# Optimization experiments

Hardware: AMD Instinct MI355X
Metric: run time of the kernel (lower is better)

The kernel has to match this reference:

```python
import jax, jax.numpy as jnp
import numpy as np
import math

B, C_IN, H, W = 8, 256, 32, 32
KDIM, OUT_CH, NUM_HEADS = 512, 512, 8


def setup_inputs() -> dict:
    key = jax.random.key(0)
    ks = jax.random.split(key, 7)
    s = 1.0 / math.sqrt(C_IN)
    inp = {
        "input": jax.random.normal(ks[0], (B, C_IN, H, W), dtype=jnp.float32),
        "q_w": jax.random.uniform(ks[1], (KDIM, C_IN), jnp.float32, -s, s),
        "q_b": jax.random.uniform(ks[2], (KDIM,), jnp.float32, -s, s),
        "k_w": jax.random.uniform(ks[3], (KDIM, C_IN), jnp.float32, -s, s),
        "k_b": jax.random.uniform(ks[4], (KDIM,), jnp.float32, -s, s),
        "v_w": jax.random.uniform(ks[5], (OUT_CH, C_IN), jnp.float32, -s, s),
        "v_b": jax.random.uniform(ks[6], (OUT_CH,), jnp.float32, -s, s),
    }
    return inp


def reference(input, q_w, q_b, k_w, k_b, v_w, v_b):
    b, c, h, w = input.shape
    s = h * w
    hd_k = KDIM // NUM_HEADS
    hd_v = OUT_CH // NUM_HEADS
    # (b, c, h, w) -> (b, s, c)
    x = jnp.transpose(input, (0, 2, 3, 1)).reshape(b, s, c)
    q = x @ q_w.T + q_b  # (b, s, kdim)
    k = x @ k_w.T + k_b  # (b, s, kdim)
    v = x @ v_w.T + v_b  # (b, s, out_ch)
    q = q.reshape(b, s, NUM_HEADS, hd_k).transpose(0, 2, 1, 3)  # (b, nh, s, hd)
    k = k.reshape(b, s, NUM_HEADS, hd_k).transpose(0, 2, 1, 3)
    v = v.reshape(b, s, NUM_HEADS, hd_v).transpose(0, 2, 1, 3)
    scores = jnp.einsum("bhqd,bhkd->bhqk", q, k) / math.sqrt(hd_k)
    causal = jnp.triu(jnp.full((s, s), -jnp.inf, dtype=scores.dtype), k=1)
    scores = scores + causal
    attn = jax.nn.softmax(scores, axis=-1)  # dropout p=0.0 -> identity
    out = jnp.einsum("bhqk,bhkd->bhqd", attn, v)  # (b, nh, s, hd_v)
    # permute(0,1,3,2) then view(b, out_ch, h, w) as in torch code
    out = out.transpose(0, 1, 3, 2).reshape(b, OUT_CH, h, w)
    return out
```

## Files before the change

### kernel.cpp

```cpp
#include <hip/hip_runtime.h>
#include <math.h>

#define BATCH 8
#define CIN 256
#define S 1024
#define KDIM 512
#define NH 8
#define HD 64

typedef float  f32x4  __attribute__((ext_vector_type(4)));
typedef short  bf16x8 __attribute__((ext_vector_type(8)));
typedef unsigned short u16x8 __attribute__((ext_vector_type(8)));

static __device__ __forceinline__ unsigned short f2bf(float x) {
    unsigned u = __builtin_bit_cast(unsigned, x);
    u += 0x7FFFu + ((u >> 16) & 1u);
    return (unsigned short)(u >> 16);
}
static __device__ __forceinline__ float bf2f(unsigned short v) {
    unsigned u = ((unsigned)v) << 16;
    return __builtin_bit_cast(float, u);
}
static __device__ __forceinline__ f32x4 mfma16(bf16x8 a, bf16x8 b, f32x4 c) {
    return __builtin_amdgcn_mfma_f32_16x16x32_bf16(a, b, c, 0, 0, 0);
}

#define PA_HI 0
#define PA_LO 8192
#define PB_HI 16384
#define PB_LO 24576

__global__ __launch_bounds__(256)
void proj_mfma_kernel(const float* __restrict__ in,
                      const float* __restrict__ q_w, const float* __restrict__ q_b,
                      const float* __restrict__ k_w, const float* __restrict__ k_b,
                      const float* __restrict__ v_w, const float* __restrict__ v_b,
                      unsigned short* __restrict__ qhi, unsigned short* __restrict__ qlo,
                      unsigned short* __restrict__ khi, unsigned short* __restrict__ klo,
                      unsigned short* __restrict__ vhi, unsigned short* __restrict__ vlo)
{
    __shared__ __attribute__((aligned(16))) char smem[32768];

    const int s0  = blockIdx.x * 128;
    const int nt  = blockIdx.y;
    const int b   = blockIdx.z;
    const int p   = nt >> 2;
    const int nb0 = (nt & 3) * 128;

    const float* w  = (p == 0) ? q_w : (p == 1) ? k_w : v_w;
    const float* bs = (p == 0) ? q_b : (p == 1) ? k_b : v_b;
    unsigned short* ph_g = (p == 0) ? qhi : (p == 1) ? khi : vhi;
    unsigned short* pl_g = (p == 0) ? qlo : (p == 1) ? klo : vlo;

    const int tid = threadIdx.x;
    const int wv  = tid >> 6;
    const int wm  = wv >> 1, wn = wv & 1;
    const int l   = tid & 63;
    const int lg  = l >> 4;
    const int lm  = l & 15;

    const float* inb = in + (size_t)b * CIN * S;

    f32x4 acc[4][4];
    #pragma unroll
    for (int mf = 0; mf < 4; ++mf)
        #pragma unroll
        for (int nf = 0; nf < 4; ++nf) acc[mf][nf] = (f32x4){0.f, 0.f, 0.f, 0.f};

    for (int c0 = 0; c0 < CIN; c0 += 32) {
        __syncthreads();
        #pragma unroll
        for (int j = 0; j < 2; ++j) {
            const int cell = tid + j * 256;
            const int m  = cell & 127;
            const int kg = cell >> 7;
            const float* src = inb + (size_t)(c0 + kg * 8) * S + s0 + m;
            u16x8 hv, lv;
            #pragma unroll
            for (int e = 0; e < 8; ++e) {
                const float v = src[(size_t)e * S];
                const unsigned short h = f2bf(v);
                hv[e] = h;
                lv[e] = f2bf(v - bf2f(h));
            }
            const int idx = (kg * 1024 + m * 8) * 2;
            *(u16x8*)(smem + PA_HI + idx) = hv;
            *(u16x8*)(smem + PA_LO + idx) = lv;
        }
        #pragma unroll
        for (int j = 0; j < 2; ++j) {
            const int cell = tid + j * 256;
            const int n  = cell & 127;
            const int kg = cell >> 7;
            const float* src = w + (size_t)(nb0 + n) * CIN + c0 + kg * 8;
            const float4 w0 = *(const float4*)src;
            const float4 w1 = *(const float4*)(src + 4);
            const float vv[8] = {w0.x, w0.y, w0.z, w0.w, w1.x, w1.y, w1.z, w1.w};
            u16x8 hv, lv;
            #pragma unroll
            for (int e = 0; e < 8; ++e) {
                const unsigned short h = f2bf(vv[e]);
                hv[e] = h;
                lv[e] = f2bf(vv[e] - bf2f(h));
            }
            const int idx = (kg * 1024 + n * 8) * 2;
            *(u16x8*)(smem + PB_HI + idx) = hv;
            *(u16x8*)(smem + PB_LO + idx) = lv;
        }
        __syncthreads();

        bf16x8 ah[4], al[4];
        #pragma unroll
        for (int mf = 0; mf < 4; ++mf) {
            const int idx = (lg * 1024 + (wm * 64 + mf * 16 + lm) * 8) * 2;
            ah[mf] = *(const bf16x8*)(smem + PA_HI + idx);
            al[mf] = *(const bf16x8*)(smem + PA_LO + idx);
        }
        __builtin_amdgcn_s_setprio(1);
        #pragma unroll
        for (int nf = 0; nf < 4; ++nf) {
            const int idx = (lg * 1024 + (wn * 64 + nf * 16 + lm) * 8) * 2;
            const bf16x8 bh = *(const bf16x8*)(smem + PB_HI + idx);
            const bf16x8 bl = *(const bf16x8*)(smem + PB_LO + idx);
            #pragma unroll
            for (int mf = 0; mf < 4; ++mf) {
                acc[mf][nf] = mfma16(ah[mf], bh, acc[mf][nf]);
                acc[mf][nf] = mfma16(al[mf], bh, acc[mf][nf]);
                acc[mf][nf] = mfma16(ah[mf], bl, acc[mf][nf]);
            }
        }
        __builtin_amdgcn_s_setprio(0);
    }

    #pragma unroll
    for (int nf = 0; nf < 4; ++nf) {
        const int ncol = nb0 + wn * 64 + nf * 16 + lm;
        const int h = ncol >> 6, d = ncol & 63;
        const float bias = bs[ncol];
        const size_t hb = ((size_t)b * NH + h) * S * HD + d;
        #pragma unroll
        for (int mf = 0; mf < 4; ++mf) {
            #pragma unroll
            for (int r = 0; r < 4; ++r) {
                const int srow = s0 + wm * 64 + mf * 16 + lg * 4 + r;
                const float x = acc[mf][nf][r] + bias;
                const unsigned short hq = f2bf(x);
                const unsigned short lq = f2bf(x - bf2f(hq));
                ph_g[hb + (size_t)srow * HD] = hq;
                pl_g[hb + (size_t)srow * HD] = lq;
            }
        }
    }
}

#define KHI_OFF  0
#define KLO_OFF  8192
#define VTHI_OFF 16384
#define VTLO_OFF 24576
#define PSHI_OFF 32768
#define PSLO_OFF 40960

__global__ __launch_bounds__(256)
void attn_mfma_kernel(const unsigned short* __restrict__ qhi_g,
                      const unsigned short* __restrict__ qlo_g,
                      const unsigned short* __restrict__ khi_g,
                      const unsigned short* __restrict__ klo_g,
                      const unsigned short* __restrict__ vhi_g,
                      const unsigned short* __restrict__ vlo_g,
                      float* __restrict__ out)
{
    __shared__ __attribute__((aligned(16))) char smem[49152];

    const int qt = 15 - (int)blockIdx.x;
    const int h  = blockIdx.y;
    const int b  = blockIdx.z;
    const int tid = threadIdx.x;
    const int w  = tid >> 6;
    const int l  = tid & 63;
    const int lg = l >> 4;
    const int lm = l & 15;
    const int s0 = qt * 64;

    const size_t base = ((size_t)b * NH + h) * S * HD;

    bf16x8 qh[2], ql[2];
    {
        const size_t qoff = base + (size_t)(s0 + w * 16 + lm) * HD + lg * 8;
        qh[0] = *(const bf16x8*)(qhi_g + qoff);
        qh[1] = *(const bf16x8*)(qhi_g + qoff + 32);
        ql[0] = *(const bf16x8*)(qlo_g + qoff);
        ql[1] = *(const bf16x8*)(qlo_g + qoff + 32);
    }

    float m[4] = {-1e30f, -1e30f, -1e30f, -1e30f};
    float lsum[4] = {0.f, 0.f, 0.f, 0.f};
    f32x4 accO[4];
    #pragma unroll
    for (int dt = 0; dt < 4; ++dt) accO[dt] = (f32x4){0.f, 0.f, 0.f, 0.f};

    for (int kt = 0; kt <= qt; ++kt) {
        __syncthreads();
        {
            const size_t kbase = base + (size_t)(kt * 64) * HD;
            #pragma unroll
            for (int i = 0; i < 2; ++i) {
                const int c = tid + i * 256;
                const int krow = c >> 3;
                const int d0 = (c & 7) * 8;
                const int swzk = (krow & 7) << 4;
                const size_t goff = kbase + (size_t)krow * HD + d0;
                const uint4 hk = *(const uint4*)(khi_g + goff);
                const uint4 lk = *(const uint4*)(klo_g + goff);
                *(uint4*)(smem + KHI_OFF + krow * 128 + ((d0 * 2) ^ swzk)) = hk;
                *(uint4*)(smem + KLO_OFF + krow * 128 + ((d0 * 2) ^ swzk)) = lk;
                const uint4 hv = *(const uint4*)(vhi_g + goff);
                const uint4 lv = *(const uint4*)(vlo_g + goff);
                const unsigned short* he = (const unsigned short*)&hv;
                const unsigned short* le = (const unsigned short*)&lv;
                #pragma unroll
                for (int j = 0; j < 8; ++j) {
                    const int d = d0 + j;
                    const int swzv = (((d >> 3) ^ d) & 7) << 4;
                    const int boff = d * 128 + ((2 * krow) ^ swzv);
                    *(unsigned short*)(smem + VTHI_OFF + boff) = he[j];
                    *(unsigned short*)(smem + VTLO_OFF + boff) = le[j];
                }
            }
        }
        __syncthreads();

        f32x4 sc[4];
        __builtin_amdgcn_s_setprio(1);
        #pragma unroll
        for (int kb = 0; kb < 4; ++kb) {
            f32x4 a = (f32x4){0.f, 0.f, 0.f, 0.f};
            #pragma unroll
            for (int ks = 0; ks < 2; ++ks) {
                const int row = kb * 16 + lm;
                const int cb = 64 * ks + 16 * lg;
                const int swz = (row & 7) << 4;
                const bf16x8 bh_ = *(const bf16x8*)(smem + KHI_OFF + row * 128 + (cb ^ swz));
                const bf16x8 bl_ = *(const bf16x8*)(smem + KLO_OFF + row * 128 + (cb ^ swz));
                a = mfma16(qh[ks], bh_, a);
                a = mfma16(ql[ks], bh_, a);
                a = mfma16(qh[ks], bl_, a);
            }
            sc[kb] = a;
        }
        __builtin_amdgcn_s_setprio(0);

        const bool diag = (kt == qt);
        float tmax[4] = {-1e30f, -1e30f, -1e30f, -1e30f};
        #pragma unroll
        for (int kb = 0; kb < 4; ++kb) {
            const int key = kt * 64 + kb * 16 + lm;
            #pragma unroll
            for (int r = 0; r < 4; ++r) {
                float v = sc[kb][r] * 0.125f;
                const int row = s0 + w * 16 + lg * 4 + r;
                if (diag && key > row) v = -1e30f;
                sc[kb][r] = v;
                tmax[r] = fmaxf(tmax[r], v);
            }
        }
        #pragma unroll
        for (int mk = 1; mk < 16; mk <<= 1)
            #pragma unroll
            for (int r = 0; r < 4; ++r)
                tmax[r] = fmaxf(tmax[r], __shfl_xor(tmax[r], mk));

        float tsum[4], sscale[4];
        #pragma unroll
        for (int r = 0; r < 4; ++r) {
            const float mn = fmaxf(m[r], tmax[r]);
            sscale[r] = __expf(m[r] - mn);
            m[r] = mn;
            float ssum = 0.f;
            #pragma unroll
            for (int kb = 0; kb < 4; ++kb) {
                const float p = __expf(sc[kb][r] - mn);
                sc[kb][r] = p;
                ssum += p;
            }
            tsum[r] = ssum;
        }
        #pragma unroll
        for (int mk = 1; mk < 16; mk <<= 1)
            #pragma unroll
            for (int r = 0; r < 4; ++r)
                tsum[r] += __shfl_xor(tsum[r], mk);

        #pragma unroll
        for (int r = 0; r < 4; ++r) {
            lsum[r] = lsum[r] * sscale[r] + tsum[r];
            #pragma unroll
            for (int dt = 0; dt < 4; ++dt) accO[dt][r] *= sscale[r];
            const int r_loc = lg * 4 + r;
            const int swz = (r_loc & 7) << 4;
            #pragma unroll
            for (int kb = 0; kb < 4; ++kb) {
                const float p = sc[kb][r];
                const unsigned short phq = f2bf(p);
                const unsigned short plq = f2bf(p - bf2f(phq));
                const int boff = (w << 11) + r_loc * 128 + ((2 * (kb * 16 + lm)) ^ swz);
                *(unsigned short*)(smem + PSHI_OFF + boff) = phq;
                *(unsigned short*)(smem + PSLO_OFF + boff) = plq;
            }
        }

        __builtin_amdgcn_s_setprio(1);
        #pragma unroll
        for (int ks = 0; ks < 2; ++ks) {
            const int cb = 64 * ks + 16 * lg;
            const int swzp = (lm & 7) << 4;
            const bf16x8 phi = *(const bf16x8*)(smem + PSHI_OFF + (w << 11) + lm * 128 + (cb ^ swzp));
            const bf16x8 plo = *(const bf16x8*)(smem + PSLO_OFF + (w << 11) + lm * 128 + (cb ^ swzp));
            #pragma unroll
            for (int dt = 0; dt < 4; ++dt) {
                const int d = dt * 16 + lm;
                const int swzv = (((d >> 3) ^ d) & 7) << 4;
                const bf16x8 vh_ = *(const bf16x8*)(smem + VTHI_OFF + d * 128 + (cb ^ swzv));
                const bf16x8 vl_ = *(const bf16x8*)(smem + VTLO_OFF + d * 128 + (cb ^ swzv));
                accO[dt] = mfma16(phi, vh_, accO[dt]);
                accO[dt] = mfma16(plo, vh_, accO[dt]);
                accO[dt] = mfma16(phi, vl_, accO[dt]);
            }
        }
        __builtin_amdgcn_s_setprio(0);
    }

    __syncthreads();
    float* Ot = (float*)smem;
    float invl[4];
    #pragma unroll
    for (int r = 0; r < 4; ++r) invl[r] = 1.0f / lsum[r];
    #pragma unroll
    for (int dt = 0; dt < 4; ++dt)
        #pragma unroll
        for (int r = 0; r < 4; ++r)
            Ot[(w * 16 + lg * 4 + r) * 66 + dt * 16 + lm] = accO[dt][r] * invl[r];
    __syncthreads();
    float* op = out + ((size_t)b * KDIM + (size_t)h * HD) * S + s0;
    #pragma unroll
    for (int i = 0; i < 16; ++i) {
        const int lin = tid + i * 256;
        const int d = lin >> 6, s = lin & 63;
        op[(size_t)d * S + s] = Ot[s * 66 + d];
    }
}

extern "C" void kernel_launch(void* const* d_in, const int* in_sizes, int n_in,
                              void* d_out, int out_size, void* d_ws, size_t ws_size,
                              hipStream_t stream)
{
    const float* input = (const float*)d_in[0];
    const float* q_w   = (const float*)d_in[1];
    const float* q_b   = (const float*)d_in[2];
    const float* k_w   = (const float*)d_in[3];
    const float* k_b   = (const float*)d_in[4];
    const float* v_w   = (const float*)d_in[5];
    const float* v_b   = (const float*)d_in[6];
    float* out = (float*)d_out;

    const size_t per = (size_t)BATCH * NH * S * HD;
    unsigned short* qhi = (unsigned short*)d_ws;
    unsigned short* qlo = qhi + per;
    unsigned short* khi = qlo + per;
    unsigned short* klo = khi + per;
    unsigned short* vhi = klo + per;
    unsigned short* vlo = vhi + per;

    proj_mfma_kernel<<<dim3(8, 12, BATCH), 256, 0, stream>>>(
        input, q_w, q_b, k_w, k_b, v_w, v_b, qhi, qlo, khi, klo, vhi, vlo);

    attn_mfma_kernel<<<dim3(S / 64, NH, BATCH), 256, 0, stream>>>(
        qhi, qlo, khi, klo, vhi, vlo, out);
}
```

Baseline: 205.6 us.

## Pre-split inputs to bf16, pair causal tiles per block, prefetch K/V

New kernels split x and the weights into bf16 hi/lo once, in a tile-friendly layout, using the output buffer as scratch. The projection then reads MFMA operands straight from global memory and no longer converts through LDS every k-step. The attention kernel gives each block two query tiles (bx and 15-bx) to balance causal work. It also register-prefetches the next K/V tile while the current one is computed. The trade-offs are extra launches, global-load latency in the projection, and reliance on the output buffer being large enough for the scratch data.

```diff
diff --git a/kernel.cpp b/kernel.cpp
--- a/kernel.cpp
+++ b/kernel.cpp
@@ -25,29 +25,94 @@
     return __builtin_amdgcn_mfma_f32_16x16x32_bf16(a, b, c, 0, 0, 0);
 }
 
-#define PA_HI 0
-#define PA_LO 8192
-#define PB_HI 16384
-#define PB_LO 24576
-
 __global__ __launch_bounds__(256)
-void proj_mfma_kernel(const float* __restrict__ in,
-                      const float* __restrict__ q_w, const float* __restrict__ q_b,
-                      const float* __restrict__ k_w, const float* __restrict__ k_b,
-                      const float* __restrict__ v_w, const float* __restrict__ v_b,
+void convert_x_kernel(const float* __restrict__ in,
+                      unsigned short* __restrict__ xt_hi,
+                      unsigned short* __restrict__ xt_lo)
+{
+    __shared__ unsigned short Hs[32][132];
+    __shared__ unsigned short Ls[32][132];
+    const int s0 = blockIdx.x * 128;
+    const int kb = blockIdx.y;
+    const int b  = blockIdx.z;
+    const int tid = threadIdx.x;
+    const float* src = in + ((size_t)b * CIN + kb * 32) * S;
+    #pragma unroll
+    for (int it = 0; it < 16; ++it) {
+        const int lin = it * 256 + tid;
+        const int c = lin >> 7;
+        const int s = lin & 127;
+        const float v = src[(size_t)c * S + s0 + s];
+        const unsigned short h = f2bf(v);
+        Hs[c][s] = h;
+        Ls[c][s] = f2bf(v - bf2f(h));
+    }
+    __syncthreads();
+    const size_t obase = ((size_t)b * 8 + kb) * (size_t)S * 32;
+    #pragma unroll
+    for (int it = 0; it < 2; ++it) {
+        const int lin = it * 256 + tid;
+        const int j = lin >> 2;
+        const int q = lin & 3;
+        u16x8 hv, lv;
+        #pragma unroll
+        for (int e = 0; e < 8; ++e) {
+            hv[e] = Hs[q * 8 + e][j];
+            lv[e] = Ls[q * 8 + e][j];
+        }
+        const size_t o = obase + (size_t)(s0 + j) * 32 + q * 8;
+        *(u16x8*)(xt_hi + o) = hv;
+        *(u16x8*)(xt_lo + o) = lv;
+    }
+}
+
+__global__ __launch_bounds__(256)
+void convert_w_kernel(const float* __restrict__ q_w, const float* __restrict__ k_w,
+                      const float* __restrict__ v_w,
+                      unsigned short* __restrict__ wt_hi,
+                      unsigned short* __restrict__ wt_lo)
+{
+    const int t = blockIdx.x * 256 + threadIdx.x;
+    const int n1536 = t >> 5;
+    const int c0 = (t & 31) * 8;
+    const int p = n1536 >> 9;
+    const int n = n1536 & 511;
+    const int kb = c0 >> 5;
+    const int cc = c0 & 31;
+    const float* w = (p == 0) ? q_w : (p == 1) ? k_w : v_w;
+    const float* src = w + (size_t)n * CIN + c0;
+    const float4 a = *(const float4*)src;
+    const float4 bq = *(const float4*)(src + 4);
+    const float vv[8] = {a.x, a.y, a.z, a.w, bq.x, bq.y, bq.z, bq.w};
+    u16x8 hv, lv;
+    #pragma unroll
+    for (int e = 0; e < 8; ++e) {
+        const unsigned short h = f2bf(vv[e]);
+        hv[e] = h;
+        lv[e] = f2bf(vv[e] - bf2f(h));
+    }
+    const size_t o = ((size_t)((p * 8 + kb) * 512 + n)) * 32 + cc;
+    *(u16x8*)(wt_hi + o) = hv;
+    *(u16x8*)(wt_lo + o) = lv;
+}
+
+__global__ __launch_bounds__(256)
+void proj_mfma_kernel(const unsigned short* __restrict__ xt_hi,
+                      const unsigned short* __restrict__ xt_lo,
+                      const unsigned short* __restrict__ wt_hi,
+                      const unsigned short* __restrict__ wt_lo,
+                      const float* __restrict__ q_b, const float* __restrict__ k_b,
+                      const float* __restrict__ v_b,
                       unsigned short* __restrict__ qhi, unsigned short* __restrict__ qlo,
                       unsigned short* __restrict__ khi, unsigned short* __restrict__ klo,
                       unsigned short* __restrict__ vhi, unsigned short* __restrict__ vlo)
 {
-    __shared__ __attribute__((aligned(16))) char smem[32768];
-
     const int s0  = blockIdx.x * 128;
     const int nt  = blockIdx.y;
     const int b   = blockIdx.z;
     const int p   = nt >> 2;
     const int nb0 = (nt & 3) * 128;
 
-    const float* w  = (p == 0) ? q_w : (p == 1) ? k_w : v_w;
     const float* bs = (p == 0) ? q_b : (p == 1) ? k_b : v_b;
     unsigned short* ph_g = (p == 0) ? qhi : (p == 1) ? khi : vhi;
     unsigned short* pl_g = (p == 0) ? qlo : (p == 1) ? klo : vlo;
@@ -59,69 +124,26 @@
     const int lg  = l >> 4;
     const int lm  = l & 15;
 
-    const float* inb = in + (size_t)b * CIN * S;
-
     f32x4 acc[4][4];
     #pragma unroll
     for (int mf = 0; mf < 4; ++mf)
         #pragma unroll
         for (int nf = 0; nf < 4; ++nf) acc[mf][nf] = (f32x4){0.f, 0.f, 0.f, 0.f};
 
-    for (int c0 = 0; c0 < CIN; c0 += 32) {
-        __syncthreads();
-        #pragma unroll
-        for (int j = 0; j < 2; ++j) {
-            const int cell = tid + j * 256;
-            const int m  = cell & 127;
-            const int kg = cell >> 7;
-            const float* src = inb + (size_t)(c0 + kg * 8) * S + s0 + m;
-            u16x8 hv, lv;
-            #pragma unroll
-            for (int e = 0; e < 8; ++e) {
-                const float v = src[(size_t)e * S];
-                const unsigned short h = f2bf(v);
-                hv[e] = h;
-                lv[e] = f2bf(v - bf2f(h));
-            }
-            const int idx = (kg * 1024 + m * 8) * 2;
-            *(u16x8*)(smem + PA_HI + idx) = hv;
-            *(u16x8*)(smem + PA_LO + idx) = lv;
-        }
-        #pragma unroll
-        for (int j = 0; j < 2; ++j) {
-            const int cell = tid + j * 256;
-            const int n  = cell & 127;
-            const int kg = cell >> 7;
-            const float* src = w + (size_t)(nb0 + n) * CIN + c0 + kg * 8;
-            const float4 w0 = *(const float4*)src;
-            const float4 w1 = *(const float4*)(src + 4);
-            const float vv[8] = {w0.x, w0.y, w0.z, w0.w, w1.x, w1.y, w1.z, w1.w};
-            u16x8 hv, lv;
-            #pragma unroll
-            for (int e = 0; e < 8; ++e) {
-                const unsigned short h = f2bf(vv[e]);
-                hv[e] = h;
-                lv[e] = f2bf(vv[e] - bf2f(h));
-            }
-            const int idx = (kg * 1024 + n * 8) * 2;
-            *(u16x8*)(smem + PB_HI + idx) = hv;
-            *(u16x8*)(smem + PB_LO + idx) = lv;
-        }
-        __syncthreads();
-
+    for (int kb = 0; kb < 8; ++kb) {
+        const size_t aoff = ((size_t)(b * 8 + kb) * S + (s0 + wm * 64 + lm)) * 32 + lg * 8;
         bf16x8 ah[4], al[4];
         #pragma unroll
         for (int mf = 0; mf < 4; ++mf) {
-            const int idx = (lg * 1024 + (wm * 64 + mf * 16 + lm) * 8) * 2;
-            ah[mf] = *(const bf16x8*)(smem + PA_HI + idx);
-            al[mf] = *(const bf16x8*)(smem + PA_LO + idx);
-        }
+            ah[mf] = *(const bf16x8*)(xt_hi + aoff + (size_t)mf * 512);
+            al[mf] = *(const bf16x8*)(xt_lo + aoff + (size_t)mf * 512);
+        }
+        const size_t boff = ((size_t)((p * 8 + kb) * 512) + (nb0 + wn * 64 + lm)) * 32 + lg * 8;
         __builtin_amdgcn_s_setprio(1);
         #pragma unroll
         for (int nf = 0; nf < 4; ++nf) {
-            const int idx = (lg * 1024 + (wn * 64 + nf * 16 + lm) * 8) * 2;
-            const bf16x8 bh = *(const bf16x8*)(smem + PB_HI + idx);
-            const bf16x8 bl = *(const bf16x8*)(smem + PB_LO + idx);
+            const bf16x8 bh = *(const bf16x8*)(wt_hi + boff + (size_t)nf * 512);
+            const bf16x8 bl = *(const bf16x8*)(wt_lo + boff + (size_t)nf * 512);
             #pragma unroll
             for (int mf = 0; mf < 4; ++mf) {
                 acc[mf][nf] = mfma16(ah[mf], bh, acc[mf][nf]);
@@ -171,7 +193,7 @@
 {
     __shared__ __attribute__((aligned(16))) char smem[49152];
 
-    const int qt = 15 - (int)blockIdx.x;
+    const int bx = blockIdx.x;
     const int h  = blockIdx.y;
     const int b  = blockIdx.z;
     const int tid = threadIdx.x;
@@ -179,44 +201,53 @@
     const int l  = tid & 63;
     const int lg = l >> 4;
     const int lm = l & 15;
-    const int s0 = qt * 64;
 
     const size_t base = ((size_t)b * NH + h) * S * HD;
 
-    bf16x8 qh[2], ql[2];
-    {
-        const size_t qoff = base + (size_t)(s0 + w * 16 + lm) * HD + lg * 8;
-        qh[0] = *(const bf16x8*)(qhi_g + qoff);
-        qh[1] = *(const bf16x8*)(qhi_g + qoff + 32);
-        ql[0] = *(const bf16x8*)(qlo_g + qoff);
-        ql[1] = *(const bf16x8*)(qlo_g + qoff + 32);
-    }
-
-    float m[4] = {-1e30f, -1e30f, -1e30f, -1e30f};
-    float lsum[4] = {0.f, 0.f, 0.f, 0.f};
-    f32x4 accO[4];
-    #pragma unroll
-    for (int dt = 0; dt < 4; ++dt) accO[dt] = (f32x4){0.f, 0.f, 0.f, 0.f};
-
-    for (int kt = 0; kt <= qt; ++kt) {
-        __syncthreads();
+    for (int pi = 0; pi < 2; ++pi) {
+        const int qt = pi ? 15 - bx : bx;
+        const int s0 = qt * 64;
+
+        bf16x8 qh[2], ql[2];
         {
-            const size_t kbase = base + (size_t)(kt * 64) * HD;
+            const size_t qoff = base + (size_t)(s0 + w * 16 + lm) * HD + lg * 8;
+            qh[0] = *(const bf16x8*)(qhi_g + qoff);
+            qh[1] = *(const bf16x8*)(qhi_g + qoff + 32);
+            ql[0] = *(const bf16x8*)(qlo_g + qoff);
+            ql[1] = *(const bf16x8*)(qlo_g + qoff + 32);
+        }
+
+        float m[4] = {-1e30f, -1e30f, -1e30f, -1e30f};
+        float lsum[4] = {0.f, 0.f, 0.f, 0.f};
+        f32x4 accO[4];
+        #pragma unroll
+        for (int dt = 0; dt < 4; ++dt) accO[dt] = (f32x4){0.f, 0.f, 0.f, 0.f};
+
+        uint4 hk[2], lk[2], hv[2], lv[2];
+        #pragma unroll
+        for (int i = 0; i < 2; ++i) {
+            const int c = tid + i * 256;
+            const int krow = c >> 3;
+            const int d0 = (c & 7) * 8;
+            const size_t goff = base + (size_t)krow * HD + d0;
+            hk[i] = *(const uint4*)(khi_g + goff);
+            lk[i] = *(const uint4*)(klo_g + goff);
+            hv[i] = *(const uint4*)(vhi_g + goff);
+            lv[i] = *(const uint4*)(vlo_g + goff);
+        }
+
+        for (int kt = 0; kt <= qt; ++kt) {
+            __syncthreads();
             #pragma unroll
             for (int i = 0; i < 2; ++i) {
                 const int c = tid + i * 256;
                 const int krow = c >> 3;
                 const int d0 = (c & 7) * 8;
                 const int swzk = (krow & 7) << 4;
-                const size_t goff = kbase + (size_t)krow * HD + d0;
-                const uint4 hk = *(const uint4*)(khi_g + goff);
-                const uint4 lk = *(const uint4*)(klo_g + goff);
-                *(uint4*)(smem + KHI_OFF + krow * 128 + ((d0 * 2) ^ swzk)) = hk;
-                *(uint4*)(smem + KLO_OFF + krow * 128 + ((d0 * 2) ^ swzk)) = lk;
-                const uint4 hv = *(const uint4*)(vhi_g + goff);
-                const uint4 lv = *(const uint4*)(vlo_g + goff);
-                const unsigned short* he = (const unsigned short*)&hv;
-                const unsigned short* le = (const unsigned short*)&lv;
+                *(uint4*)(smem + KHI_OFF + krow * 128 + ((d0 * 2) ^ swzk)) = hk[i];
+                *(uint4*)(smem + KLO_OFF + krow * 128 + ((d0 * 2) ^ swzk)) = lk[i];
+                const unsigned short* he = (const unsigned short*)&hv[i];
+                const unsigned short* le = (const unsigned short*)&lv[i];
                 #pragma unroll
                 for (int j = 0; j < 8; ++j) {
                     const int d = d0 + j;
@@ -226,126 +257,141 @@
                     *(unsigned short*)(smem + VTLO_OFF + boff) = le[j];
                 }
             }
-        }
+            if (kt < qt) {
+                const size_t kbase = base + (size_t)((kt + 1) * 64) * HD;
+                #pragma unroll
+                for (int i = 0; i < 2; ++i) {
+                    const int c = tid + i * 256;
+                    const int krow = c >> 3;
+                    const int d0 = (c & 7) * 8;
+                    const size_t goff = kbase + (size_t)krow * HD + d0;
+                    hk[i] = *(const uint4*)(khi_g + goff);
+                    lk[i] = *(const uint4*)(klo_g + goff);
+                    hv[i] = *(const uint4*)(vhi_g + goff);
+                    lv[i] = *(const uint4*)(vlo_g + goff);
+                }
+            }
+            __syncthreads();
+
+            f32x4 sc[4];
+            __builtin_amdgcn_s_setprio(1);
+            #pragma unroll
+            for (int kb = 0; kb < 4; ++kb) {
+                f32x4 a = (f32x4){0.f, 0.f, 0.f, 0.f};
+                #pragma unroll
+                for (int ks = 0; ks < 2; ++ks) {
+                    const int row = kb * 16 + lm;
+                    const int cb = 64 * ks + 16 * lg;
+                    const int swz = (row & 7) << 4;
+                    const bf16x8 bh_ = *(const bf16x8*)(smem + KHI_OFF + row * 128 + (cb ^ swz));
+                    const bf16x8 bl_ = *(const bf16x8*)(smem + KLO_OFF + row * 128 + (cb ^ swz));
+                    a = mfma16(qh[ks], bh_, a);
+                    a = mfma16(ql[ks], bh_, a);
+                    a = mfma16(qh[ks], bl_, a);
+                }
+                sc[kb] = a;
+            }
+            __builtin_amdgcn_s_setprio(0);
+
+            const bool diag = (kt == qt);
+            float tmax[4] = {-1e30f, -1e30f, -1e30f, -1e30f};
+            #pragma unroll
+            for (int kb = 0; kb < 4; ++kb) {
+                const int key = kt * 64 + kb * 16 + lm;
+                #pragma unroll
+                for (int r = 0; r < 4; ++r) {
+                    float v = sc[kb][r] * 0.125f;
+                    const int row = s0 + w * 16 + lg * 4 + r;
+                    if (diag && key > row) v = -1e30f;
+                    sc[kb][r] = v;
+                    tmax[r] = fmaxf(tmax[r], v);
+                }
+            }
+            #pragma unroll
+            for (int mk = 1; mk < 16; mk <<= 1)
+                #pragma unroll
+                for (int r = 0; r < 4; ++r)
+                    tmax[r] = fmaxf(tmax[r], __shfl_xor(tmax[r], mk));
+
+            float tsum[4], sscale[4];
+            #pragma unroll
+            for (int r = 0; r < 4; ++r) {
+                const float mn = fmaxf(m[r], tmax[r]);
+                sscale[r] = __expf(m[r] - mn);
+                m[r] = mn;
+                float ssum = 0.f;
+                #pragma unroll
+                for (int kb = 0; kb < 4; ++kb) {
+                    const float p = __expf(sc[kb][r] - mn);
+                    sc[kb][r] = p;
+                    ssum += p;
+                }
+                tsum[r] = ssum;
+            }
+            #pragma unroll
+            for (int mk = 1; mk < 16; mk <<= 1)
+                #pragma unroll
+                for (int r = 0; r < 4; ++r)
+                    tsum[r] += __shfl_xor(tsum[r], mk);
+
+            #pragma unroll
+            for (int r = 0; r < 4; ++r) {
+                lsum[r] = lsum[r] * sscale[r] + tsum[r];
+                #pragma unroll
+                for (int dt = 0; dt < 4; ++dt) accO[dt][r] *= sscale[r];
+                const int r_loc = lg * 4 + r;
+                const int swz = (r_loc & 7) << 4;
+                #pragma unroll
+                for (int kb = 0; kb < 4; ++kb) {
+                    const float p = sc[kb][r];
+                    const unsigned short phq = f2bf(p);
+                    const unsigned short plq = f2bf(p - bf2f(phq));
+                    const int boff = (w << 11) + r_loc * 128 + ((2 * (kb * 16 + lm)) ^ swz);
+                    *(unsigned short*)(smem + PSHI_OFF + boff) = phq;
+                    *(unsigned short*)(smem + PSLO_OFF + boff) = plq;
+                }
+            }
+
+            __builtin_amdgcn_s_setprio(1);
+            #pragma unroll
+            for (int ks = 0; ks < 2; ++ks) {
+                const int cb = 64 * ks + 16 * lg;
+                const int swzp = (lm & 7) << 4;
+                const bf16x8 phi = *(const bf16x8*)(smem + PSHI_OFF + (w << 11) + lm * 128 + (cb ^ swzp));
+                const bf16x8 plo = *(const bf16x8*)(smem + PSLO_OFF + (w << 11) + lm * 128 + (cb ^ swzp));
+                #pragma unroll
+                for (int dt = 0; dt < 4; ++dt) {
+                    const int d = dt * 16 + lm;
+                    const int swzv = (((d >> 3) ^ d) & 7) << 4;
+                    const bf16x8 vh_ = *(const bf16x8*)(smem + VTHI_OFF + d * 128 + (cb ^ swzv));
+                    const bf16x8 vl_ = *(const bf16x8*)(smem + VTLO_OFF + d * 128 + (cb ^ swzv));
+                    accO[dt] = mfma16(phi, vh_, accO[dt]);
+                    accO[dt] = mfma16(plo, vh_, accO[dt]);
+                    accO[dt] = mfma16(phi, vl_, accO[dt]);
+                }
+            }
+            __builtin_amdgcn_s_setprio(0);
+        }
+
         __syncthreads();
-
-        f32x4 sc[4];
-        __builtin_amdgcn_s_setprio(1);
-        #pragma unroll
-        for (int kb = 0; kb < 4; ++kb) {
-            f32x4 a = (f32x4){0.f, 0.f, 0.f, 0.f};
-            #pragma unroll
-            for (int ks = 0; ks < 2; ++ks) {
-                const int row = kb * 16 + lm;
-                const int cb = 64 * ks + 16 * lg;
-                const int swz = (row & 7) << 4;
-                const bf16x8 bh_ = *(const bf16x8*)(smem + KHI_OFF + row * 128 + (cb ^ swz));
-                const bf16x8 bl_ = *(const bf16x8*)(smem + KLO_OFF + row * 128 + (cb ^ swz));
-                a = mfma16(qh[ks], bh_, a);
-                a = mfma16(ql[ks], bh_, a);
-                a = mfma16(qh[ks], bl_, a);
-            }
-            sc[kb] = a;
-        }
-        __builtin_amdgcn_s_setprio(0);
-
-        const bool diag = (kt == qt);
-        float tmax[4] = {-1e30f, -1e30f, -1e30f, -1e30f};
-        #pragma unroll
-        for (int kb = 0; kb < 4; ++kb) {
-            const int key = kt * 64 + kb * 16 + lm;
-            #pragma unroll
-            for (int r = 0; r < 4; ++r) {
-                float v = sc[kb][r] * 0.125f;
-                const int row = s0 + w * 16 + lg * 4 + r;
-                if (diag && key > row) v = -1e30f;
-                sc[kb][r] = v;
-                tmax[r] = fmaxf(tmax[r], v);
-            }
-        }
-        #pragma unroll
-        for (int mk = 1; mk < 16; mk <<= 1)
+        float* Ot = (float*)smem;
+        float invl[4];
+        #pragma unroll
+        for (int r = 0; r < 4; ++r) invl[r] = 1.0f / lsum[r];
+        #pragma unroll
+        for (int dt = 0; dt < 4; ++dt)
             #pragma unroll
             for (int r = 0; r < 4; ++r)
-                tmax[r] = fmaxf(tmax[r], __shfl_xor(tmax[r], mk));
-
-        float tsum[4], sscale[4];
-        #pragma unroll
-        for (int r = 0; r < 4; ++r) {
-            const float mn = fmaxf(m[r], tmax[r]);
-            sscale[r] = __expf(m[r] - mn);
-            m[r] = mn;
-            float ssum = 0.f;
-            #pragma unroll
-            for (int kb = 0; kb < 4; ++kb) {
-                const float p = __expf(sc[kb][r] - mn);
-                sc[kb][r] = p;
-                ssum += p;
-            }
-            tsum[r] = ssum;
-        }
-        #pragma unroll
-        for (int mk = 1; mk < 16; mk <<= 1)
-            #pragma unroll
-            for (int r = 0; r < 4; ++r)
-                tsum[r] += __shfl_xor(tsum[r], mk);
-
-        #pragma unroll
-        for (int r = 0; r < 4; ++r) {
-            lsum[r] = lsum[r] * sscale[r] + tsum[r];
-            #pragma unroll
-            for (int dt = 0; dt < 4; ++dt) accO[dt][r] *= sscale[r];
-            const int r_loc = lg * 4 + r;
-            const int swz = (r_loc & 7) << 4;
-            #pragma unroll
-            for (int kb = 0; kb < 4; ++kb) {
-                const float p = sc[kb][r];
-                const unsigned short phq = f2bf(p);
-                const unsigned short plq = f2bf(p - bf2f(phq));
-                const int boff = (w << 11) + r_loc * 128 + ((2 * (kb * 16 + lm)) ^ swz);
-                *(unsigned short*)(smem + PSHI_OFF + boff) = phq;
-                *(unsigned short*)(smem + PSLO_OFF + boff) = plq;
-            }
-        }
-
-        __builtin_amdgcn_s_setprio(1);
-        #pragma unroll
-        for (int ks = 0; ks < 2; ++ks) {
-            const int cb = 64 * ks + 16 * lg;
-            const int swzp = (lm & 7) << 4;
-            const bf16x8 phi = *(const bf16x8*)(smem + PSHI_OFF + (w << 11) + lm * 128 + (cb ^ swzp));
-            const bf16x8 plo = *(const bf16x8*)(smem + PSLO_OFF + (w << 11) + lm * 128 + (cb ^ swzp));
-            #pragma unroll
-            for (int dt = 0; dt < 4; ++dt) {
-                const int d = dt * 16 + lm;
-                const int swzv = (((d >> 3) ^ d) & 7) << 4;
-                const bf16x8 vh_ = *(const bf16x8*)(smem + VTHI_OFF + d * 128 + (cb ^ swzv));
-                const bf16x8 vl_ = *(const bf16x8*)(smem + VTLO_OFF + d * 128 + (cb ^ swzv));
-                accO[dt] = mfma16(phi, vh_, accO[dt]);
-                accO[dt] = mfma16(plo, vh_, accO[dt]);
-                accO[dt] = mfma16(phi, vl_, accO[dt]);
-            }
-        }
-        __builtin_amdgcn_s_setprio(0);
-    }
-
-    __syncthreads();
-    float* Ot = (float*)smem;
-    float invl[4];
-    #pragma unroll
-    for (int r = 0; r < 4; ++r) invl[r] = 1.0f / lsum[r];
-    #pragma unroll
-    for (int dt = 0; dt < 4; ++dt)
-        #pragma unroll
-        for (int r = 0; r < 4; ++r)
-            Ot[(w * 16 + lg * 4 + r) * 66 + dt * 16 + lm] = accO[dt][r] * invl[r];
-    __syncthreads();
-    float* op = out + ((size_t)b * KDIM + (size_t)h * HD) * S + s0;
-    #pragma unroll
-    for (int i = 0; i < 16; ++i) {
-        const int lin = tid + i * 256;
-        const int d = lin >> 6, s = lin & 63;
-        op[(size_t)d * S + s] = Ot[s * 66 + d];
+                Ot[(w * 16 + lg * 4 + r) * 66 + dt * 16 + lm] = accO[dt][r] * invl[r];
+        __syncthreads();
+        float* op = out + ((size_t)b * KDIM + (size_t)h * HD) * S + s0;
+        #pragma unroll
+        for (int i = 0; i < 16; ++i) {
+            const int lin = tid + i * 256;
+            const int d = lin >> 6, s = lin & 63;
+            op[(size_t)d * S + s] = Ot[s * 66 + d];
+        }
+        __syncthreads();
     }
 }
 
@@ -370,9 +416,18 @@
     unsigned short* vhi = klo + per;
     unsigned short* vlo = vhi + per;
 
+    unsigned short* xt_hi = (unsigned short*)d_out;
+    unsigned short* xt_lo = xt_hi + (size_t)BATCH * CIN * S;
+    unsigned short* wt_hi = xt_lo + (size_t)BATCH * CIN * S;
+    unsigned short* wt_lo = wt_hi + (size_t)3 * KDIM * CIN;
+
+    convert_x_kernel<<<dim3(8, 8, BATCH), 256, 0, stream>>>(input, xt_hi, xt_lo);
+    convert_w_kernel<<<dim3(192, 1, 1), 256, 0, stream>>>(q_w, k_w, v_w, wt_hi, wt_lo);
+
     proj_mfma_kernel<<<dim3(8, 12, BATCH), 256, 0, stream>>>(
-        input, q_w, q_b, k_w, k_b, v_w, v_b, qhi, qlo, khi, klo, vhi, vlo);
-
-    attn_mfma_kernel<<<dim3(S / 64, NH, BATCH), 256, 0, stream>>>(
+        xt_hi, xt_lo, wt_hi, wt_lo, q_b, k_b, v_b,
+        qhi, qlo, khi, klo, vhi, vlo);
+
+    attn_mfma_kernel<<<dim3(8, NH, BATCH), 256, 0, stream>>>(
         qhi, qlo, khi, klo, vhi, vlo, out);
 }
```

Result: faster. 195.9 us (-4.7%).
